# Optimization experiments

Hardware: AMD Instinct MI355X
Metric: run time of the kernel (lower is better)

## Reference

```python
import jax, jax.numpy as jnp
import numpy as np

B, C, H, W = 8, 64, 128, 128


def _conv3x3(x, w, b):
    # x: [B,C,H,W], w: [O,I,3,3], b: [O]; stride 1, padding 1
    y = jax.lax.conv_general_dilated(
        x, w, window_strides=(1, 1), padding=((1, 1), (1, 1)),
        dimension_numbers=('NCHW', 'OIHW', 'NCHW'))
    return y + b[None, :, None, None]


def setup_inputs() -> dict:
    key = jax.random.key(0)
    ks = jax.random.split(key, 8)
    s = 0.05
    return {
        'x': jax.random.normal(ks[0], (B, C, H, W), jnp.float32),
        'Wq': jax.random.normal(ks[1], (C, C, 3, 3), jnp.float32) * s,
        'bq': jax.random.normal(ks[2], (C,), jnp.float32) * s,
        'Wk': jax.random.normal(ks[3], (C, C, 3, 3), jnp.float32) * s,
        'bk': jax.random.normal(ks[4], (C,), jnp.float32) * s,
        'Wv': jax.random.normal(ks[5], (C, C, 3, 3), jnp.float32) * s,
        'bv': jax.random.normal(ks[6], (C,), jnp.float32) * s,
        'gamma': jax.random.normal(ks[7], (1,), jnp.float32) * s,
    }


def reference(x, Wq, bq, Wk, bk, Wv, bv, gamma):
    b_, c_, h_, w_ = x.shape
    q = _conv3x3(x, Wq, bq)  # [B,C,H,W]
    k = _conv3x3(x, Wk, bk)
    v = _conv3x3(x, Wv, bv)

    # energy along H (column attention): eH[b,h,w,g] = sum_c q[b,c,h,w]*k[b,c,g,w]
    eH = jnp.einsum('bchw,bcgw->bhwg', q, k)
    eye = jnp.eye(h_, dtype=bool)  # mask diagonal h==g with -inf
    eH = jnp.where(eye[None, :, None, :], -jnp.inf, eH)

    # energy along W (row attention): eW[b,h,w,g] = sum_c q[b,c,h,w]*k[b,c,h,g]
    eW = jnp.einsum('bchw,bchg->bhwg', q, k)

    # joint softmax over concatenated [H | W] axis
    att = jax.nn.softmax(jnp.concatenate([eH, eW], axis=3), axis=3)
    att_H = att[:, :, :, :h_]          # [B,H,W,H]
    att_W = att[:, :, :, h_:h_ + w_]   # [B,H,W,W]

    out_H = jnp.einsum('bcgw,bhwg->bchw', v, att_H)
    out_W = jnp.einsum('bchg,bhwg->bchw', v, att_W)

    return gamma[0] * (out_H + out_W) + x
```

## Files before the change

### kernel.cpp

```cpp
#include <hip/hip_runtime.h>
#include <hip/hip_bf16.h>

#define B_ 8
#define C_ 64
#define H_ 128
#define W_ 128
#define HW_  ((size_t)H_ * W_)
#define CHW_ ((size_t)C_ * H_ * W_)

typedef unsigned short u16;
typedef unsigned int   u32;
typedef __attribute__((ext_vector_type(8))) short bf16x8;
typedef __attribute__((ext_vector_type(4))) float f32x4;

__device__ __forceinline__ float bf2f(u16 h) {
    union { u32 u; float f; } c; c.u = ((u32)h) << 16; return c.f;
}
__device__ __forceinline__ u16 f2bf(float f) {
    union { float f; u32 u; } c; c.f = f;
    u32 u = c.u;
    u32 r = (u + 0x7fffu + ((u >> 16) & 1u)) >> 16;
    return (u16)r;
}
__device__ __forceinline__ u32 pack2(float a, float b) {
    return (u32)f2bf(a) | ((u32)f2bf(b) << 16);
}
__device__ __forceinline__ float sanit(float x, float lo, float hi) {
    return fminf(fmaxf(x, lo), hi);
}
__device__ __forceinline__ void gload_lds16(const u16* g, u16* l) {
    __builtin_amdgcn_global_load_lds(
        (const __attribute__((address_space(1))) void*)g,
        (__attribute__((address_space(3))) void*)l, 16, 0, 0);
}

__global__ __launch_bounds__(256) void prep_weights(
    const float* __restrict__ Wq, const float* __restrict__ Wk,
    const float* __restrict__ Wv, u16* __restrict__ Wt)
{
    int tap = blockIdx.x;
    int cog = blockIdx.y * 4 + (threadIdx.x >> 6);
    int ci  = threadIdx.x & 63;
    int arr = cog >> 6, co = cog & 63;
    const float* src = arr == 0 ? Wq : (arr == 1 ? Wk : Wv);
    Wt[tap * 12288 + cog * 64 + ci] = f2bf(src[(co * 64 + ci) * 9 + tap]);
}

__global__ __launch_bounds__(256) void xprep_kernel(
    const float* __restrict__ x, u16* __restrict__ xb)
{
    const int hp  = blockIdx.x;
    const int tid = threadIdx.x;
    u16* dst = xb + ((size_t)blockIdx.y * 130 + hp) * 8192;
    if (hp == 0 || hp == 129) {
#pragma unroll
        for (int i = 0; i < 4; i++)
            *(uint4*)(dst + (size_t)(tid + i * 256) * 8) = (uint4){0, 0, 0, 0};
        return;
    }
    const float* xr = x + (size_t)blockIdx.y * CHW_ + (size_t)(hp - 1) * W_;
#pragma unroll
    for (int it = 0; it < 4; it++) {
        int idx = tid + it * 256;
        int px  = idx & 127;
        int g   = idx >> 7;
        float vb[8];
#pragma unroll
        for (int e = 0; e < 8; e++)
            vb[e] = xr[(size_t)(g * 8 + e) * HW_ + px];
        uint4 o;
        o.x = pack2(vb[0], vb[1]);
        o.y = pack2(vb[2], vb[3]);
        o.z = pack2(vb[4], vb[5]);
        o.w = pack2(vb[6], vb[7]);
        *(uint4*)(dst + (size_t)(g * 128 + px) * 8) = o;
    }
}

__global__ __launch_bounds__(256, 2) void conv_mfma_kernel(
    const u16* __restrict__ xb, const u16* __restrict__ Wt,
    const float* __restrict__ bq, const float* __restrict__ bk,
    const float* __restrict__ bv,
    u16* __restrict__ qN, u16* __restrict__ kN, u16* __restrict__ v)
{
    const int nwg  = gridDim.x * gridDim.y;
    const int flat = blockIdx.y * gridDim.x + blockIdx.x;
    const int wg   = (flat & 7) * (nwg >> 3) + (flat >> 3);
    const int p    = wg & 1;
    const int hq   = (wg >> 1) & 31;
    const int bidx = wg >> 6;
    const int h0   = hq * 4;
    const size_t boff = (size_t)bidx * CHW_;
    const int tid  = threadIdx.x;
    const int lane = tid & 63, wv = tid >> 6;
    const int ln15 = lane & 15, quad = lane >> 4;

    __shared__ __align__(16) u16 xI[26112];

    const int woff = (wv * 16 + ln15) * 64 + quad * 8;

    const u16* xrow0 = xb + ((size_t)bidx * 130 + h0) * 8192;
#pragma unroll
    for (int it = 0; it < 12; it++) {
        int unit = wv * 12 + it;
        int i = unit >> 3, g = unit & 7;
        const u16* src = xrow0 + (size_t)i * 8192 + g * 1024 + p * 512 - 16;
        u16* dst = xI + (i * 8 + g) * 544;
        gload_lds16(src + lane * 8, dst);
        gload_lds16(src + 32 + lane * 8, dst + 32);
    }
    __syncthreads();
    if (tid < 48) {
        int i = tid >> 3, g = tid & 7;
        int slot = p ? 66 : 1;
        *(uint4*)(xI + (i * 8 + g) * 544 + slot * 8) = (uint4){0, 0, 0, 0};
    }
    __syncthreads();

    const int cb = wv * 16 + quad * 4;
    float bqv[4], bkv[4], bvv[4];
#pragma unroll
    for (int r = 0; r < 4; r++) {
        bqv[r] = bq[cb + r]; bkv[r] = bk[cb + r]; bvv[r] = bv[cb + r];
    }

#pragma unroll
    for (int pass = 0; pass < 2; pass++) {
        f32x4 acc[2][3][4];
#pragma unroll
        for (int hh = 0; hh < 2; hh++)
#pragma unroll
            for (int mt = 0; mt < 3; mt++)
#pragma unroll
                for (int nt = 0; nt < 4; nt++)
                    acc[hh][mt][nt] = (f32x4){0.f, 0.f, 0.f, 0.f};

        bf16x8 wcur[2][3], wnxt[2][3];
#pragma unroll
        for (int ks = 0; ks < 2; ks++)
#pragma unroll
            for (int mt = 0; mt < 3; mt++)
                wcur[ks][mt] = *(const bf16x8*)(Wt + woff + mt * 4096 + ks * 32);

#pragma unroll
        for (int tap = 0; tap < 9; tap++) {
            const int dh = tap / 3, dw = tap % 3;
            if (tap < 8) {
#pragma unroll
                for (int ks = 0; ks < 2; ks++)
#pragma unroll
                    for (int mt = 0; mt < 3; mt++)
                        wnxt[ks][mt] = *(const bf16x8*)(Wt + (tap + 1) * 12288 + woff + mt * 4096 + ks * 32);
            }
#pragma unroll
            for (int hh = 0; hh < 2; hh++) {
                const int row = pass * 2 + hh + dh;
#pragma unroll
                for (int ks = 0; ks < 2; ks++) {
                    bf16x8 bfr[4];
#pragma unroll
                    for (int nt = 0; nt < 4; nt++)
                        bfr[nt] = *(const bf16x8*)(xI + (row * 8 + quad + ks * 4) * 544
                                                      + (nt * 16 + ln15 + 1 + dw) * 8);
                    __builtin_amdgcn_s_setprio(1);
#pragma unroll
                    for (int mt = 0; mt < 3; mt++)
#pragma unroll
                        for (int nt = 0; nt < 4; nt++)
                            acc[hh][mt][nt] = __builtin_amdgcn_mfma_f32_16x16x32_bf16(
                                wcur[ks][mt], bfr[nt], acc[hh][mt][nt], 0, 0, 0);
                    __builtin_amdgcn_s_setprio(0);
                }
            }
            if (tap < 8) {
#pragma unroll
                for (int ks = 0; ks < 2; ks++)
#pragma unroll
                    for (int mt = 0; mt < 3; mt++)
                        wcur[ks][mt] = wnxt[ks][mt];
            }
        }

#pragma unroll
        for (int hh = 0; hh < 2; hh++) {
            const int h = h0 + pass * 2 + hh;
#pragma unroll
            for (int mt = 0; mt < 2; mt++) {
                const float* bb = mt == 0 ? bqv : bkv;
                u16* dst = (mt ? kN : qN) + boff + (size_t)h * W_ * 64 + cb;
#pragma unroll
                for (int nt = 0; nt < 4; nt++) {
                    int px = p * 64 + nt * 16 + ln15;
                    u32 p0 = pack2(acc[hh][mt][nt][0] + bb[0], acc[hh][mt][nt][1] + bb[1]);
                    u32 p1 = pack2(acc[hh][mt][nt][2] + bb[2], acc[hh][mt][nt][3] + bb[3]);
                    *(u32*)(dst + (size_t)px * 64)     = p0;
                    *(u32*)(dst + (size_t)px * 64 + 2) = p1;
                }
            }
#pragma unroll
            for (int r = 0; r < 4; r++) {
                u16* drow = v + boff + (size_t)(cb + r) * HW_ + (size_t)h * W_;
#pragma unroll
                for (int nt = 0; nt < 4; nt++)
                    drow[p * 64 + nt * 16 + ln15] = f2bf(acc[hh][2][nt][r] + bvv[r]);
            }
        }
    }
}

__global__ __launch_bounds__(256) void vt_kernel(
    const u16* __restrict__ v, u16* __restrict__ vT)
{
    __shared__ u16 Ts[64 * 72];
    const u16* src = v  + (size_t)blockIdx.z * CHW_ + (size_t)blockIdx.y * HW_;
    u16* dst       = vT + (size_t)blockIdx.z * CHW_ + (size_t)blockIdx.y * HW_;
    const int ti = blockIdx.x & 1, tj = blockIdx.x >> 1;
    const int r0 = ti * 64, c0 = tj * 64;
    const int tid = threadIdx.x;
    const int r = tid >> 2, cq = tid & 3;
#pragma unroll
    for (int i = 0; i < 2; i++) {
        uint4 u = *(const uint4*)(src + (size_t)(r0 + r) * 128 + c0 + cq * 16 + i * 8);
        *(uint4*)(Ts + r * 72 + cq * 16 + i * 8) = u;
    }
    __syncthreads();
    const int wr = tid >> 2, hq = tid & 3;
    union { u16 o[16]; uint4 v4[2]; } t;
#pragma unroll
    for (int j = 0; j < 16; j++) t.o[j] = Ts[(hq * 16 + j) * 72 + wr];
    *(uint4*)(dst + (size_t)(c0 + wr) * 128 + r0 + hq * 16)     = t.v4[0];
    *(uint4*)(dst + (size_t)(c0 + wr) * 128 + r0 + hq * 16 + 8) = t.v4[1];
}

__global__ __launch_bounds__(256, 4) void col_kernel(
    const u16* __restrict__ qN, const u16* __restrict__ kN,
    const u16* __restrict__ vT,
    float* __restrict__ maxH, float* __restrict__ sumH,
    u16* __restrict__ Ocol)
{
    const size_t boff = (size_t)blockIdx.z * CHW_;
    const size_t soff = (size_t)blockIdx.z * HW_;
    qN += boff; kN += boff; vT += boff; Ocol += boff;
    maxH += soff; sumH += soff;

    const int s    = blockIdx.x;
    const int tid  = threadIdx.x;
    const int lane = tid & 63, wv = tid >> 6;
    const int ln15 = lane & 15, quad = lane >> 4;

    __shared__ __align__(16) u16 smemU[18432];
    u16* Qs = smemU;
    u16* Ks = smemU + 9216;

#pragma unroll
    for (int it = 0; it < 4; it++) {
        int idx = tid + it * 256;
        int t = idx >> 3, cg = (idx & 7) * 8;
        size_t off = (size_t)t * 8192 + (size_t)s * 64 + cg;
        *(uint4*)(Qs + t * 72 + cg) = *(const uint4*)(qN + off);
        *(uint4*)(Ks + t * 72 + cg) = *(const uint4*)(kN + off);
    }
    __syncthreads();

    f32x4 Sc[2][8];
#pragma unroll
    for (int tt = 0; tt < 2; tt++)
#pragma unroll
        for (int gt = 0; gt < 8; gt++)
            Sc[tt][gt] = (f32x4){0.f, 0.f, 0.f, 0.f};

#pragma unroll
    for (int ks = 0; ks < 2; ks++) {
        bf16x8 bq_[2];
#pragma unroll
        for (int tt = 0; tt < 2; tt++)
            bq_[tt] = *(const bf16x8*)(Qs + ((wv * 2 + tt) * 16 + ln15) * 72 + ks * 32 + quad * 8);
#pragma unroll
        for (int gt = 0; gt < 8; gt++) {
            bf16x8 ak = *(const bf16x8*)(Ks + (gt * 16 + ln15) * 72 + ks * 32 + quad * 8);
#pragma unroll
            for (int tt = 0; tt < 2; tt++)
                Sc[tt][gt] = __builtin_amdgcn_mfma_f32_16x16x32_bf16(ak, bq_[tt], Sc[tt][gt], 0, 0, 0);
        }
    }

    const int tb[2] = { (wv * 2) * 16 + ln15, (wv * 2 + 1) * 16 + ln15 };
#pragma unroll
    for (int tt = 0; tt < 2; tt++)
#pragma unroll
        for (int gt = 0; gt < 8; gt++)
#pragma unroll
            for (int r = 0; r < 4; r++)
                if (gt * 16 + quad * 4 + r == tb[tt]) Sc[tt][gt][r] = -1e30f;

#pragma unroll
    for (int tt = 0; tt < 2; tt++) {
        float m = Sc[tt][0][0];
#pragma unroll
        for (int gt = 0; gt < 8; gt++)
#pragma unroll
            for (int r = 0; r < 4; r++) m = fmaxf(m, Sc[tt][gt][r]);
        m = fmaxf(m, __shfl_xor(m, 16));
        m = fmaxf(m, __shfl_xor(m, 32));
        float ss = 0.f;
#pragma unroll
        for (int gt = 0; gt < 8; gt++)
#pragma unroll
            for (int r = 0; r < 4; r++) {
                float e = __expf(Sc[tt][gt][r] - m);
                ss += e;
                Sc[tt][gt][r] = e;
            }
        ss += __shfl_xor(ss, 16);
        ss += __shfl_xor(ss, 32);
        if (quad == 0) {
            int pix = tb[tt] * W_ + s;
            maxH[pix] = m; sumH[pix] = ss;
        }
    }
    __syncthreads();
    u16* Ps = smemU;
#pragma unroll
    for (int tt = 0; tt < 2; tt++)
#pragma unroll
        for (int gt = 0; gt < 8; gt++) {
            u32 lo = pack2(Sc[tt][gt][0], Sc[tt][gt][1]);
            u32 hi = pack2(Sc[tt][gt][2], Sc[tt][gt][3]);
            *(uint2*)(Ps + tb[tt] * 136 + gt * 16 + quad * 4) = make_uint2(lo, hi);
        }
    __syncthreads();

    f32x4 Oc[2][4];
#pragma unroll
    for (int mt = 0; mt < 2; mt++)
#pragma unroll
        for (int nt = 0; nt < 4; nt++)
            Oc[mt][nt] = (f32x4){0.f, 0.f, 0.f, 0.f};
#pragma unroll
    for (int kg = 0; kg < 4; kg++) {
        bf16x8 ap[2];
#pragma unroll
        for (int mt = 0; mt < 2; mt++)
            ap[mt] = *(const bf16x8*)(Ps + (wv * 32 + mt * 16 + ln15) * 136 + kg * 32 + quad * 8);
#pragma unroll
        for (int nt = 0; nt < 4; nt++) {
            bf16x8 bv_ = *(const bf16x8*)(vT + (size_t)(nt * 16 + ln15) * HW_ + (size_t)s * 128 + kg * 32 + quad * 8);
#pragma unroll
            for (int mt = 0; mt < 2; mt++)
                Oc[mt][nt] = __builtin_amdgcn_mfma_f32_16x16x32_bf16(ap[mt], bv_, Oc[mt][nt], 0, 0, 0);
        }
    }
    __syncthreads();
    u16* OfU = smemU;
#pragma unroll
    for (int mt = 0; mt < 2; mt++)
#pragma unroll
        for (int nt = 0; nt < 4; nt++)
#pragma unroll
            for (int r = 0; r < 4; r++)
                OfU[(wv * 32 + mt * 16 + quad * 4 + r) * 72 + nt * 16 + ln15] = f2bf(Oc[mt][nt][r]);
    __syncthreads();
#pragma unroll
    for (int it = 0; it < 4; it++) {
        int idx = tid + it * 256;
        int t = idx >> 3, c8 = (idx & 7) * 8;
        *(uint4*)(Ocol + ((size_t)t * 128 + s) * 64 + c8) = *(uint4*)(OfU + t * 72 + c8);
    }
}

__global__ __launch_bounds__(256, 4) void row_kernel(
    const u16* __restrict__ qN, const u16* __restrict__ kN,
    const u16* __restrict__ v,
    const float* __restrict__ x, const float* __restrict__ gammap,
    const float* __restrict__ maxH, const float* __restrict__ sumH,
    const u16* __restrict__ Ocol, float* __restrict__ out)
{
    const size_t boff = (size_t)blockIdx.z * CHW_;
    const size_t soff = (size_t)blockIdx.z * HW_;
    qN += boff; kN += boff; v += boff; Ocol += boff; x += boff; out += boff;
    maxH += soff; sumH += soff;

    const int s    = blockIdx.x;
    const int tid  = threadIdx.x;
    const int lane = tid & 63, wv = tid >> 6;
    const int ln15 = lane & 15, quad = lane >> 4;

    __shared__ __align__(16) u16 smemU[18432];
    u16* Qs = smemU;
    u16* Ks = smemU + 9216;
    float* alL = (float*)(smemU + 17408);

    const int tb[2] = { (wv * 2) * 16 + ln15, (wv * 2 + 1) * 16 + ln15 };
    float mcv[2], scv[2];
#pragma unroll
    for (int tt = 0; tt < 2; tt++) {
        mcv[tt] = maxH[s * W_ + tb[tt]];
        scv[tt] = sumH[s * W_ + tb[tt]];
    }

#pragma unroll
    for (int it = 0; it < 4; it++) {
        int idx = tid + it * 256;
        int t = idx >> 3, cg = (idx & 7) * 8;
        size_t off = (size_t)s * 8192 + (size_t)t * 64 + cg;
        *(uint4*)(Qs + t * 72 + cg) = *(const uint4*)(qN + off);
        *(uint4*)(Ks + t * 72 + cg) = *(const uint4*)(kN + off);
    }
    __syncthreads();

    f32x4 Sc[2][8];
#pragma unroll
    for (int tt = 0; tt < 2; tt++)
#pragma unroll
        for (int gt = 0; gt < 8; gt++)
            Sc[tt][gt] = (f32x4){0.f, 0.f, 0.f, 0.f};
#pragma unroll
    for (int ks = 0; ks < 2; ks++) {
        bf16x8 bq_[2];
#pragma unroll
        for (int tt = 0; tt < 2; tt++)
            bq_[tt] = *(const bf16x8*)(Qs + ((wv * 2 + tt) * 16 + ln15) * 72 + ks * 32 + quad * 8);
#pragma unroll
        for (int gt = 0; gt < 8; gt++) {
            bf16x8 ak = *(const bf16x8*)(Ks + (gt * 16 + ln15) * 72 + ks * 32 + quad * 8);
#pragma unroll
            for (int tt = 0; tt < 2; tt++)
                Sc[tt][gt] = __builtin_amdgcn_mfma_f32_16x16x32_bf16(ak, bq_[tt], Sc[tt][gt], 0, 0, 0);
        }
    }

    float be[2];
#pragma unroll
    for (int tt = 0; tt < 2; tt++) {
        float m = Sc[tt][0][0];
#pragma unroll
        for (int gt = 0; gt < 8; gt++)
#pragma unroll
            for (int r = 0; r < 4; r++) m = fmaxf(m, Sc[tt][gt][r]);
        m = fmaxf(m, __shfl_xor(m, 16));
        m = fmaxf(m, __shfl_xor(m, 32));
        float ss = 0.f;
#pragma unroll
        for (int gt = 0; gt < 8; gt++)
#pragma unroll
            for (int r = 0; r < 4; r++) {
                float e = __expf(Sc[tt][gt][r] - m);
                ss += e;
                Sc[tt][gt][r] = e;
            }
        ss += __shfl_xor(ss, 16);
        ss += __shfl_xor(ss, 32);
        float mc = sanit(mcv[tt], -3e38f, 3e38f);
        float sc = sanit(scv[tt], 0.f, 3e38f);
        float mm = fmaxf(mc, m);
        float dd = sc * __expf(fminf(mc - mm, 0.f)) + ss * __expf(m - mm);
        float rv = 1.0f / fmaxf(dd, 1e-30f);
        be[tt] = __expf(m - mm) * rv;
        if (quad == 0) alL[tb[tt]] = __expf(fminf(mc - mm, 0.f)) * rv;
    }
    __syncthreads();
    u16* Ps = smemU;
#pragma unroll
    for (int tt = 0; tt < 2; tt++)
#pragma unroll
        for (int gt = 0; gt < 8; gt++) {
            u32 lo = pack2(Sc[tt][gt][0] * be[tt], Sc[tt][gt][1] * be[tt]);
            u32 hi = pack2(Sc[tt][gt][2] * be[tt], Sc[tt][gt][3] * be[tt]);
            *(uint2*)(Ps + tb[tt] * 136 + gt * 16 + quad * 4) = make_uint2(lo, hi);
        }
    __syncthreads();

    f32x4 Oc[2][4];
#pragma unroll
    for (int mt = 0; mt < 2; mt++)
#pragma unroll
        for (int nt = 0; nt < 4; nt++)
            Oc[mt][nt] = (f32x4){0.f, 0.f, 0.f, 0.f};
#pragma unroll
    for (int kg = 0; kg < 4; kg++) {
        bf16x8 ap[2];
#pragma unroll
        for (int mt = 0; mt < 2; mt++)
            ap[mt] = *(const bf16x8*)(Ps + (wv * 32 + mt * 16 + ln15) * 136 + kg * 32 + quad * 8);
#pragma unroll
        for (int nt = 0; nt < 4; nt++) {
            bf16x8 bv_ = *(const bf16x8*)(v + (size_t)(nt * 16 + ln15) * HW_ + (size_t)s * 128 + kg * 32 + quad * 8);
#pragma unroll
            for (int mt = 0; mt < 2; mt++)
                Oc[mt][nt] = __builtin_amdgcn_mfma_f32_16x16x32_bf16(ap[mt], bv_, Oc[mt][nt], 0, 0, 0);
        }
    }
    __syncthreads();

    const float gmm = gammap[0];
    float* Of = (float*)smemU;
#pragma unroll
    for (int mt = 0; mt < 2; mt++)
#pragma unroll
        for (int nt = 0; nt < 4; nt++) {
            float fv[4];
            int c = nt * 16 + ln15;
#pragma unroll
            for (int r = 0; r < 4; r++) {
                int tt = wv * 32 + mt * 16 + quad * 4 + r;
                float oc = bf2f(Ocol[((size_t)s * 128 + tt) * 64 + c]);
                fv[r] = gmm * (Oc[mt][nt][r] + alL[tt] * oc);
            }
            int w0 = wv * 32 + mt * 16 + quad * 4;
            *(float4*)(Of + c * 132 + w0) = make_float4(fv[0], fv[1], fv[2], fv[3]);
        }
    __syncthreads();
    int c = tid >> 2, w0 = (tid & 3) * 32;
#pragma unroll
    for (int i = 0; i < 8; i++) {
        int w = w0 + i * 4;
        float4 xo = *(const float4*)(x + (size_t)c * HW_ + (size_t)s * 128 + w);
        float4 of = *(const float4*)(Of + c * 132 + w);
        *(float4*)(out + (size_t)c * HW_ + (size_t)s * 128 + w) =
            make_float4(of.x + xo.x, of.y + xo.y, of.z + xo.z, of.w + xo.w);
    }
}

extern "C" void kernel_launch(void* const* d_in, const int* in_sizes, int n_in,
                              void* d_out, int out_size, void* d_ws, size_t ws_size,
                              hipStream_t stream)
{
    const float* x  = (const float*)d_in[0];
    const float* Wq = (const float*)d_in[1];
    const float* bq = (const float*)d_in[2];
    const float* Wk = (const float*)d_in[3];
    const float* bk = (const float*)d_in[4];
    const float* Wv = (const float*)d_in[5];
    const float* bv = (const float*)d_in[6];
    const float* gm = (const float*)d_in[7];
    float* out = (float*)d_out;

    char* ws = (char*)d_ws;
    const size_t need1 = 4 * (size_t)B_ * CHW_ * 2 + (size_t)B_ * CHW_ * 4
                       + 2 * (size_t)B_ * HW_ * 4 + 221184;
    int passes = (ws_size >= need1) ? 1 : 2;
    int nb = B_ / passes;

    const size_t SL = (size_t)nb * CHW_ * 2;
    const size_t OC = (size_t)nb * CHW_ * 4;
    const size_t ST = (size_t)nb * HW_ * 4;
    u16*   qNb  = (u16*)(ws);
    u16*   kNb  = (u16*)(ws + SL);
    u16*   v    = (u16*)(ws + 2 * SL);
    u16*   vT   = (u16*)(ws + 3 * SL);
    u16*   Ocol = (u16*)(ws + 4 * SL);
    float* maxH = (float*)(ws + 4 * SL + OC);
    float* sumH = (float*)(ws + 4 * SL + OC + ST);
    u16*   Wt   = (u16*)(ws + 4 * SL + OC + 2 * ST);
    u16*   xb   = (u16*)Ocol;

    dim3 blk(256);
    prep_weights<<<dim3(9, 48), blk, 0, stream>>>(Wq, Wk, Wv, Wt);

    for (int p = 0; p < passes; p++) {
        const float* xbp = x + (size_t)p * nb * CHW_;
        float* ob = out + (size_t)p * nb * CHW_;
        xprep_kernel<<<dim3(130, nb), blk, 0, stream>>>(xbp, xb);
        conv_mfma_kernel<<<dim3(64, nb), blk, 0, stream>>>(xb, Wt, bq, bk, bv, qNb, kNb, v);
        vt_kernel<<<dim3(4, C_, nb), blk, 0, stream>>>(v, vT);
        col_kernel<<<dim3(W_, 1, nb), blk, 0, stream>>>(qNb, kNb, vT, maxH, sumH, Ocol);
        row_kernel<<<dim3(H_, 1, nb), blk, 0, stream>>>(qNb, kNb, v, xbp, gm, maxH, sumH, Ocol, ob);
    }
}
```

Baseline: 187.2 us.

## Fuse V transpose into conv epilogue and remap workgroup-to-tile assignment

The conv kernel now writes the transposed V tensor directly from its accumulators: it keeps the first pass's V values in registers and emits packed 4-element column chunks after the second pass. This removes the separate vt_kernel launch and its extra read and write of V. The workgroup-index mapping is also changed so that consecutive workgroups per XCD group cover different row quads, which changes L2 locality. In exchange the kernel holds 32 more floats in registers and issues narrow 8-byte strided stores for vT.

```diff
diff --git a/kernel.cpp b/kernel.cpp
--- a/kernel.cpp
+++ b/kernel.cpp
@@ -81,15 +81,18 @@
     const u16* __restrict__ xb, const u16* __restrict__ Wt,
     const float* __restrict__ bq, const float* __restrict__ bk,
     const float* __restrict__ bv,
-    u16* __restrict__ qN, u16* __restrict__ kN, u16* __restrict__ v)
+    u16* __restrict__ qN, u16* __restrict__ kN,
+    u16* __restrict__ v, u16* __restrict__ vT)
 {
-    const int nwg  = gridDim.x * gridDim.y;
-    const int flat = blockIdx.y * gridDim.x + blockIdx.x;
-    const int wg   = (flat & 7) * (nwg >> 3) + (flat >> 3);
-    const int p    = wg & 1;
-    const int hq   = (wg >> 1) & 31;
-    const int bidx = wg >> 6;
-    const int h0   = hq * 4;
+    const int nwg    = gridDim.x * gridDim.y;
+    const int flat   = blockIdx.y * gridDim.x + blockIdx.x;
+    const int groups = nwg >> 3;
+    const int m      = flat / groups;
+    const int g      = flat - m * groups;
+    const int bidx   = g >> 3;
+    const int p      = (g >> 2) & 1;
+    const int hq     = (g & 3) * 8 + m;
+    const int h0     = hq * 4;
     const size_t boff = (size_t)bidx * CHW_;
     const int tid  = threadIdx.x;
     const int lane = tid & 63, wv = tid >> 6;
@@ -103,17 +106,17 @@
 #pragma unroll
     for (int it = 0; it < 12; it++) {
         int unit = wv * 12 + it;
-        int i = unit >> 3, g = unit & 7;
-        const u16* src = xrow0 + (size_t)i * 8192 + g * 1024 + p * 512 - 16;
-        u16* dst = xI + (i * 8 + g) * 544;
+        int i = unit >> 3, gg = unit & 7;
+        const u16* src = xrow0 + (size_t)i * 8192 + gg * 1024 + p * 512 - 16;
+        u16* dst = xI + (i * 8 + gg) * 544;
         gload_lds16(src + lane * 8, dst);
         gload_lds16(src + 32 + lane * 8, dst + 32);
     }
     __syncthreads();
     if (tid < 48) {
-        int i = tid >> 3, g = tid & 7;
+        int i = tid >> 3, gg = tid & 7;
         int slot = p ? 66 : 1;
-        *(uint4*)(xI + (i * 8 + g) * 544 + slot * 8) = (uint4){0, 0, 0, 0};
+        *(uint4*)(xI + (i * 8 + gg) * 544 + slot * 8) = (uint4){0, 0, 0, 0};
     }
     __syncthreads();
 
@@ -123,6 +126,8 @@
     for (int r = 0; r < 4; r++) {
         bqv[r] = bq[cb + r]; bkv[r] = bk[cb + r]; bvv[r] = bv[cb + r];
     }
+
+    float vhold[2][4][4];
 
 #pragma unroll
     for (int pass = 0; pass < 2; pass++) {
@@ -201,35 +206,28 @@
             for (int r = 0; r < 4; r++) {
                 u16* drow = v + boff + (size_t)(cb + r) * HW_ + (size_t)h * W_;
 #pragma unroll
-                for (int nt = 0; nt < 4; nt++)
-                    drow[p * 64 + nt * 16 + ln15] = f2bf(acc[hh][2][nt][r] + bvv[r]);
-            }
-        }
-    }
-}
-
-__global__ __launch_bounds__(256) void vt_kernel(
-    const u16* __restrict__ v, u16* __restrict__ vT)
-{
-    __shared__ u16 Ts[64 * 72];
-    const u16* src = v  + (size_t)blockIdx.z * CHW_ + (size_t)blockIdx.y * HW_;
-    u16* dst       = vT + (size_t)blockIdx.z * CHW_ + (size_t)blockIdx.y * HW_;
-    const int ti = blockIdx.x & 1, tj = blockIdx.x >> 1;
-    const int r0 = ti * 64, c0 = tj * 64;
-    const int tid = threadIdx.x;
-    const int r = tid >> 2, cq = tid & 3;
-#pragma unroll
-    for (int i = 0; i < 2; i++) {
-        uint4 u = *(const uint4*)(src + (size_t)(r0 + r) * 128 + c0 + cq * 16 + i * 8);
-        *(uint4*)(Ts + r * 72 + cq * 16 + i * 8) = u;
-    }
-    __syncthreads();
-    const int wr = tid >> 2, hq = tid & 3;
-    union { u16 o[16]; uint4 v4[2]; } t;
-#pragma unroll
-    for (int j = 0; j < 16; j++) t.o[j] = Ts[(hq * 16 + j) * 72 + wr];
-    *(uint4*)(dst + (size_t)(c0 + wr) * 128 + r0 + hq * 16)     = t.v4[0];
-    *(uint4*)(dst + (size_t)(c0 + wr) * 128 + r0 + hq * 16 + 8) = t.v4[1];
+                for (int nt = 0; nt < 4; nt++) {
+                    float vb_ = acc[hh][2][nt][r] + bvv[r];
+                    drow[p * 64 + nt * 16 + ln15] = f2bf(vb_);
+                    if (pass == 0) vhold[hh][nt][r] = vb_;
+                }
+            }
+        }
+        if (pass == 1) {
+#pragma unroll
+            for (int r = 0; r < 4; r++) {
+                u16* vtc = vT + boff + (size_t)(cb + r) * HW_ + (size_t)h0;
+#pragma unroll
+                for (int nt = 0; nt < 4; nt++) {
+                    int px = p * 64 + nt * 16 + ln15;
+                    uint2 u;
+                    u.x = pack2(vhold[0][nt][r], vhold[1][nt][r]);
+                    u.y = pack2(acc[0][2][nt][r] + bvv[r], acc[1][2][nt][r] + bvv[r]);
+                    *(uint2*)(vtc + (size_t)px * 128) = u;
+                }
+            }
+        }
+    }
 }
 
 __global__ __launch_bounds__(256, 4) void col_kernel(
@@ -561,8 +559,7 @@
         const float* xbp = x + (size_t)p * nb * CHW_;
         float* ob = out + (size_t)p * nb * CHW_;
         xprep_kernel<<<dim3(130, nb), blk, 0, stream>>>(xbp, xb);
-        conv_mfma_kernel<<<dim3(64, nb), blk, 0, stream>>>(xb, Wt, bq, bk, bv, qNb, kNb, v);
-        vt_kernel<<<dim3(4, C_, nb), blk, 0, stream>>>(v, vT);
+        conv_mfma_kernel<<<dim3(64, nb), blk, 0, stream>>>(xb, Wt, bq, bk, bv, qNb, kNb, v, vT);
         col_kernel<<<dim3(W_, 1, nb), blk, 0, stream>>>(qNb, kNb, vT, maxH, sumH, Ocol);
         row_kernel<<<dim3(H_, 1, nb), blk, 0, stream>>>(qNb, kNb, v, xbp, gm, maxH, sumH, Ocol, ob);
     }
```

New measurement: 200.9 us. +7.3%, slower.
